# Kernel tuning notes

Hardware: AMD Instinct MI355X
Metric: run time of the kernel (lower is better)

The kernel has to match this reference:

```python
import jax, jax.numpy as jnp
import numpy as np

EPS = 1e-6

def _conv(x, w, padding):
    # x: [B,C,H,W], w: [O,I,kh,kw]
    return jax.lax.conv_general_dilated(x, w, window_strides=(1, 1), padding=padding,
                                        dimension_numbers=('NCHW', 'OIHW', 'NCHW'))

def setup_inputs() -> dict:
    key = jax.random.key(0)
    ks = jax.random.split(key, 8)
    C = 512
    B, H, W = 4, 64, 64
    s1 = 1.0 / np.sqrt(C)          # 1x1 conv fan-in
    s3 = 1.0 / np.sqrt(C * 9)      # 3x3 conv fan-in
    return {
        'x': jax.random.normal(ks[0], (B, C, H, W), dtype=jnp.float32),
        'ln_w': jnp.ones((C,), dtype=jnp.float32),
        'ln_b': jnp.zeros((C,), dtype=jnp.float32),
        'wq': jax.random.normal(ks[1], (C, C, 1, 1), dtype=jnp.float32) * s1,
        'wk': jax.random.normal(ks[2], (C, C, 3, 3), dtype=jnp.float32) * s3,
        'wv': jax.random.normal(ks[3], (C, C, 3, 3), dtype=jnp.float32) * s3,
        'wp': jax.random.normal(ks[4], (C, C, 1, 1), dtype=jnp.float32) * s1,
        'bp': jnp.zeros((C,), dtype=jnp.float32),
    }

def reference(x, ln_w, ln_b, wq, wk, wv, wp, bp):
    # channels_first LayerNorm over C
    u = jnp.mean(x, axis=1, keepdims=True)
    s = jnp.mean((x - u) ** 2, axis=1, keepdims=True)
    h = (x - u) / jnp.sqrt(s + EPS)
    h = ln_w[None, :, None, None] * h + ln_b[None, :, None, None]

    q = _conv(h, wq, 'VALID')           # 1x1
    k = _conv(h, wk, [(1, 1), (1, 1)])  # 3x3, pad 1
    v = _conv(h, wv, [(1, 1), (1, 1)])

    b, c, H, W = q.shape
    hw = H * W
    q = q.reshape(b, c, hw)
    k = k.reshape(b, c, hw)
    v = v.reshape(b, c, hw)

    scale = jnp.asarray(int(c) ** (-0.5), q.dtype)
    attn = jnp.einsum('bcm,bcn->bmn', q, k) * scale  # [b, hw_q, hw_k]
    attn = jax.nn.softmax(attn, axis=2)
    out = jnp.einsum('bcn,bmn->bcm', v, attn)        # [b, c, hw_q]
    out = out.reshape(b, c, H, W)

    out = _conv(out, wp, 'VALID') + bp[None, :, None, None]
    return x + out
```

## Files before the change

kernel.cpp:

```cpp
#include <hip/hip_runtime.h>
#include <hip/hip_bf16.h>

#define C_DIM 512
#define HW    4096
#define BATCH 4
#define PW    66
#define PPIX  (PW*PW)

typedef __attribute__((ext_vector_type(8))) short bf16x8;
typedef __attribute__((ext_vector_type(4))) float f32x4;
typedef __attribute__((ext_vector_type(16))) float f32x16;
typedef __attribute__((ext_vector_type(2))) long long l64x2;

static __device__ __forceinline__ short f2b(float f) {
    union { float f; unsigned u; } v; v.f = f;
    unsigned r = v.u + 0x7fffu + ((v.u >> 16) & 1u);
    return (short)(r >> 16);
}
static __device__ __forceinline__ float b2f(short s) {
    union { unsigned u; float f; } v; v.u = ((unsigned)(unsigned short)s) << 16;
    return v.f;
}

static __device__ __forceinline__ f32x4 zero4() {
    f32x4 v = {0.f, 0.f, 0.f, 0.f};
    return v;
}
static __device__ __forceinline__ f32x16 zero16() {
    f32x16 v = {0.f,0.f,0.f,0.f, 0.f,0.f,0.f,0.f, 0.f,0.f,0.f,0.f, 0.f,0.f,0.f,0.f};
    return v;
}

static __device__ __forceinline__ void gload16(const void* g, void* l) {
    __builtin_amdgcn_global_load_lds(
        (__attribute__((address_space(1))) void*)g,
        (__attribute__((address_space(3))) void*)l, 16, 0, 0);
}

__global__ void k_cvt_bf16(const float* __restrict__ in, short* __restrict__ out, int n) {
    int i = blockIdx.x * 256 + threadIdx.x;
    if (i < n) out[i] = f2b(in[i]);
}

__global__ void k_reorder_w3(const float* __restrict__ w, short* __restrict__ out) {
    int i = blockIdx.x * 256 + threadIdx.x;
    int c   = i & 511;
    int tap = (i >> 9) % 9;
    int o   = i / (9 * 512);
    out[i] = f2b(w[((size_t)o * 512 + c) * 9 + tap]);
}

__global__ void k_cvt_k8(const short* __restrict__ in, unsigned char* __restrict__ out) {
    int i = blockIdx.x * 256 + threadIdx.x;
    int m = i >> 6;
    int p = (i & 63) * 8;
    int kcp = p >> 6, g = (p >> 4) & 3, half = (p >> 3) & 1;
    int chb = (kcp * 2 + half) * 32 + g * 8;
    bf16x8 v = *(const bf16x8*)&in[(size_t)m * 512 + chb];
    int lo = __builtin_amdgcn_cvt_pk_fp8_f32(b2f(v[0]), b2f(v[1]), 0, false);
    lo     = __builtin_amdgcn_cvt_pk_fp8_f32(b2f(v[2]), b2f(v[3]), lo, true);
    int hi = __builtin_amdgcn_cvt_pk_fp8_f32(b2f(v[4]), b2f(v[5]), 0, false);
    hi     = __builtin_amdgcn_cvt_pk_fp8_f32(b2f(v[6]), b2f(v[7]), hi, true);
    *(uint2*)&out[(size_t)m * 512 + p] = make_uint2((unsigned)lo, (unsigned)hi);
}

__global__ void k_ln_stats(const float* __restrict__ x, float* __restrict__ mean,
                           float* __restrict__ rstd) {
    __shared__ float ss[8][32];
    __shared__ float sq2[8][32];
    int bid = blockIdx.x;
    int t = threadIdx.x;
    int px = t & 31, cg = t >> 5;
    int p = bid * 32 + px;
    int b = p >> 12, pix = p & 4095;
    const float* xp = x + (size_t)b * C_DIM * HW + pix;
    float s = 0.f, sq = 0.f;
    #pragma unroll 4
    for (int c = cg * 64; c < cg * 64 + 64; ++c) {
        float v = xp[(size_t)c * HW];
        s += v; sq += v * v;
    }
    ss[cg][px] = s;
    sq2[cg][px] = sq;
    __syncthreads();
    if (t < 32) {
        float S = 0.f, Q = 0.f;
        #pragma unroll
        for (int j = 0; j < 8; ++j) { S += ss[j][t]; Q += sq2[j][t]; }
        float mu  = S * (1.0f / C_DIM);
        float var = Q * (1.0f / C_DIM) - mu * mu;
        int pg = bid * 32 + t;
        mean[pg] = mu;
        rstd[pg] = 1.0f / sqrtf(var + 1e-6f);
    }
}

__global__ void k_ln_apply(const float* __restrict__ x, const float* __restrict__ mean,
                           const float* __restrict__ rstd, const float* __restrict__ lnw,
                           const float* __restrict__ lnb, short* __restrict__ hp) {
    __shared__ short tile[64][65];
    int bid = blockIdx.x;
    int ct = bid & 7, y = (bid >> 3) & 63, b = bid >> 9;
    int c0 = ct * 64, p0 = y * 64;
    int t = threadIdx.x;
    int pi = t & 63, ci0 = t >> 6;
    int pg = (b << 12) + p0 + pi;
    float mu = mean[pg], rs = rstd[pg];
    const float* xb = x + (size_t)b * C_DIM * HW;
    #pragma unroll
    for (int cc = 0; cc < 64; cc += 4) {
        int c = c0 + cc + ci0;
        float v = xb[(size_t)c * HW + p0 + pi];
        tile[cc + ci0][pi] = f2b((v - mu) * rs * lnw[c] + lnb[c]);
    }
    __syncthreads();
    int cj = t & 63, pj = t >> 6;
    #pragma unroll
    for (int pp = 0; pp < 64; pp += 4) {
        int pidx = pp + pj;
        size_t dst = ((size_t)b * PPIX + (size_t)(y + 1) * PW + 1 + pidx) * C_DIM + c0 + cj;
        hp[dst] = tile[cj][pidx];
    }
}

template<int TAPS, int GMODE, int EPI>
__global__ __launch_bounds__(256, 2) void k_gemm(
        const short* __restrict__ A, const short* __restrict__ Bw,
        void* __restrict__ Out, const float* __restrict__ bias,
        const float* __restrict__ resid)
{
    constexpr int K = TAPS * 512;
    constexpr int NKC = K / 64;
    __shared__ short Alds[128 * 64];
    __shared__ short Blds[128 * 64];
    int bid = blockIdx.x;
    int mt = bid & 31, nt = (bid >> 5) & 3, b = bid >> 7;
    int m0 = mt * 128, n0 = nt * 128;
    int t = threadIdx.x;
    int lane = t & 63, w = t >> 6;
    int wm = w >> 1, wn = w & 1;
    int g = lane >> 4, li = lane & 15;
    int srow = t >> 3, schunk = t & 7;
    const short* Ab = A + (GMODE == 0 ? (size_t)b * PPIX * C_DIM : (size_t)b * HW * C_DIM);

    f32x4 acc[4][4];
    #pragma unroll
    for (int i = 0; i < 4; ++i)
        #pragma unroll
        for (int j = 0; j < 4; ++j) acc[i][j] = zero4();

    for (int kc = 0; kc < NKC; ++kc) {
        int tap = (TAPS == 9) ? (kc >> 3) : 4;
        int cb  = (kc & 7) * 64;
        __syncthreads();
        #pragma unroll
        for (int r = 0; r < 4; ++r) {
            int row = r * 32 + srow;
            size_t goff;
            if (GMODE == 0) {
                int m = m0 + row;
                int yy = m >> 6, xx = m & 63;
                int pp = (yy + tap / 3) * PW + xx + (tap % 3);
                goff = (size_t)pp * C_DIM + cb + schunk * 8;
            } else {
                goff = (size_t)(m0 + row) * K + kc * 64 + schunk * 8;
            }
            gload16(Ab + goff, Alds + row * 64 + schunk * 8);
        }
        #pragma unroll
        for (int r = 0; r < 4; ++r) {
            int row = r * 32 + srow;
            size_t goff = (size_t)(n0 + row) * K + kc * 64 + schunk * 8;
            gload16(Bw + goff, Blds + row * 64 + schunk * 8);
        }
        __syncthreads();
        #pragma unroll
        for (int ks = 0; ks < 2; ++ks) {
            int koff = ks * 32 + g * 8;
            bf16x8 af[4], bfr[4];
            #pragma unroll
            for (int i = 0; i < 4; ++i)
                af[i] = *(const bf16x8*)&Alds[(wm * 64 + i * 16 + li) * 64 + koff];
            #pragma unroll
            for (int j = 0; j < 4; ++j)
                bfr[j] = *(const bf16x8*)&Blds[(wn * 64 + j * 16 + li) * 64 + koff];
            #pragma unroll
            for (int i = 0; i < 4; ++i)
                #pragma unroll
                for (int j = 0; j < 4; ++j)
                    acc[i][j] = __builtin_amdgcn_mfma_f32_16x16x32_bf16(af[i], bfr[j], acc[i][j], 0, 0, 0);
        }
    }
    #pragma unroll
    for (int fm = 0; fm < 4; ++fm) {
        #pragma unroll
        for (int fn = 0; fn < 4; ++fn) {
            int mrow = m0 + wm * 64 + fm * 16 + g * 4;
            int ncol = n0 + wn * 64 + fn * 16 + li;
            if constexpr (EPI == 0) {
                #pragma unroll
                for (int i = 0; i < 4; ++i) {
                    size_t dst = ((size_t)b * HW + mrow + i) * C_DIM + ncol;
                    ((short*)Out)[dst] = f2b(acc[fm][fn][i]);
                }
            } else if constexpr (EPI == 1) {
                size_t dst = ((size_t)b * C_DIM + ncol) * HW + mrow;
                short4 sv = make_short4(f2b(acc[fm][fn][0]), f2b(acc[fm][fn][1]),
                                        f2b(acc[fm][fn][2]), f2b(acc[fm][fn][3]));
                *(short4*)((short*)Out + dst) = sv;
            } else {
                size_t dst = ((size_t)b * C_DIM + ncol) * HW + mrow;
                float bb = bias[ncol];
                float4 xr = *(const float4*)(resid + dst);
                float4 o;
                o.x = acc[fm][fn][0] + bb + xr.x;
                o.y = acc[fm][fn][1] + bb + xr.y;
                o.z = acc[fm][fn][2] + bb + xr.z;
                o.w = acc[fm][fn][3] + bb + xr.w;
                *(float4*)((float*)Out + dst) = o;
            }
        }
    }
}

__global__ __launch_bounds__(256, 2) void k_gemm_kv(
        const short* __restrict__ A, const short* __restrict__ Bk,
        const short* __restrict__ Bv, short* __restrict__ OutK,
        short* __restrict__ OutV)
{
    constexpr int K = 4608;
    __shared__ short Alds[128 * 64];
    __shared__ short Bklds[128 * 64];
    __shared__ short Bvlds[128 * 64];
    int bid = blockIdx.x;
    int mt = bid & 31, nt = (bid >> 5) & 3, b = bid >> 7;
    int m0 = mt * 128, n0 = nt * 128;
    int t = threadIdx.x;
    int lane = t & 63, w = t >> 6;
    int wm = w >> 1, wn = w & 1;
    int g = lane >> 4, li = lane & 15;
    int srow = t >> 3, schunk = t & 7;
    const short* Ab = A + (size_t)b * PPIX * C_DIM;

    f32x4 accK[4][4], accV[4][4];
    #pragma unroll
    for (int i = 0; i < 4; ++i)
        #pragma unroll
        for (int j = 0; j < 4; ++j) { accK[i][j] = zero4(); accV[i][j] = zero4(); }

    for (int kc = 0; kc < 72; ++kc) {
        int tap = kc >> 3;
        int cb  = (kc & 7) * 64;
        __syncthreads();
        #pragma unroll
        for (int r = 0; r < 4; ++r) {
            int row = r * 32 + srow;
            int m = m0 + row;
            int yy = m >> 6, xx = m & 63;
            int pp = (yy + tap / 3) * PW + xx + (tap % 3);
            gload16(Ab + (size_t)pp * C_DIM + cb + schunk * 8, Alds + row * 64 + schunk * 8);
        }
        #pragma unroll
        for (int r = 0; r < 4; ++r) {
            int row = r * 32 + srow;
            size_t goff = (size_t)(n0 + row) * K + kc * 64 + schunk * 8;
            gload16(Bk + goff, Bklds + row * 64 + schunk * 8);
            gload16(Bv + goff, Bvlds + row * 64 + schunk * 8);
        }
        __syncthreads();
        #pragma unroll
        for (int ks = 0; ks < 2; ++ks) {
            int koff = ks * 32 + g * 8;
            bf16x8 af[4], bk[4], bv[4];
            #pragma unroll
            for (int i = 0; i < 4; ++i)
                af[i] = *(const bf16x8*)&Alds[(wm * 64 + i * 16 + li) * 64 + koff];
            #pragma unroll
            for (int j = 0; j < 4; ++j)
                bk[j] = *(const bf16x8*)&Bklds[(wn * 64 + j * 16 + li) * 64 + koff];
            #pragma unroll
            for (int i = 0; i < 4; ++i)
                #pragma unroll
                for (int j = 0; j < 4; ++j)
                    accK[i][j] = __builtin_amdgcn_mfma_f32_16x16x32_bf16(af[i], bk[j], accK[i][j], 0, 0, 0);
            #pragma unroll
            for (int j = 0; j < 4; ++j)
                bv[j] = *(const bf16x8*)&Bvlds[(wn * 64 + j * 16 + li) * 64 + koff];
            #pragma unroll
            for (int i = 0; i < 4; ++i)
                #pragma unroll
                for (int j = 0; j < 4; ++j)
                    accV[i][j] = __builtin_amdgcn_mfma_f32_16x16x32_bf16(af[i], bv[j], accV[i][j], 0, 0, 0);
        }
    }
    #pragma unroll
    for (int fm = 0; fm < 4; ++fm) {
        #pragma unroll
        for (int fn = 0; fn < 4; ++fn) {
            int mrow = m0 + wm * 64 + fm * 16 + g * 4;
            int ncol = n0 + wn * 64 + fn * 16 + li;
            #pragma unroll
            for (int i = 0; i < 4; ++i) {
                size_t dst = ((size_t)b * HW + mrow + i) * C_DIM + ncol;
                OutK[dst] = f2b(accK[fm][fn][i]);
            }
            size_t dstv = ((size_t)b * C_DIM + ncol) * HW + mrow;
            short4 sv = make_short4(f2b(accV[fm][fn][0]), f2b(accV[fm][fn][1]),
                                    f2b(accV[fm][fn][2]), f2b(accV[fm][fn][3]));
            *(short4*)(OutV + dstv) = sv;
        }
    }
}

#define KT 32
#define NTILES 64
__global__ __launch_bounds__(512, 2) void k_attn(
        const short* __restrict__ qT, const unsigned char* __restrict__ kT8,
        const short* __restrict__ vg, short* __restrict__ O0,
        short* __restrict__ O1, float* __restrict__ L0, float* __restrict__ L1)
{
    __shared__ __align__(16) short pool[73728];
    unsigned char* Kp8 = (unsigned char*)pool;
    short* Vp = pool + 16384;
    short* Pp = pool + 57344;

    int bid0 = blockIdx.x;
    int bid = (bid0 & 7) * 32 + (bid0 >> 3);
    int qt = bid & 31, ks = (bid >> 5) & 1, b = bid >> 6;
    int m0 = qt * 128;
    int t = threadIdx.x, lane = t & 63, w = t >> 6;
    int g = lane >> 4, li = lane & 15;
    int l31 = lane & 31, l5 = lane >> 5;

    const unsigned char* kb8 = kT8 + ((size_t)b * HW + (size_t)ks * 2048) * 512;
    const short* vb = vg + (size_t)b * C_DIM * HW + ks * 2048;

    long long qf8[16];
    {
        const short* qrow = qT + ((size_t)b * HW + m0 + w * 16 + li) * C_DIM;
        #pragma unroll
        for (int kc = 0; kc < 16; ++kc) {
            bf16x8 qv = *(const bf16x8*)&qrow[kc * 32 + g * 8];
            int lo = __builtin_amdgcn_cvt_pk_fp8_f32(b2f(qv[0]), b2f(qv[1]), 0, false);
            lo     = __builtin_amdgcn_cvt_pk_fp8_f32(b2f(qv[2]), b2f(qv[3]), lo, true);
            int hi = __builtin_amdgcn_cvt_pk_fp8_f32(b2f(qv[4]), b2f(qv[5]), 0, false);
            hi     = __builtin_amdgcn_cvt_pk_fp8_f32(b2f(qv[6]), b2f(qv[7]), hi, true);
            qf8[kc] = ((long long)(unsigned)hi << 32) | (unsigned)lo;
        }
    }
    f32x16 oacc[8];
    #pragma unroll
    for (int a = 0; a < 8; ++a) oacc[a] = zero16();
    float lsum = 0.f;

    const unsigned char* ksrc8 = kb8 + (size_t)(t & 31) * 512 + (t >> 5) * 16;
    int voff[5];
    #pragma unroll
    for (int r = 0; r < 5; ++r) {
        int D = r * 512 + t;
        int ch = D / 5;
        int c  = D - ch * 5;
        voff[r] = (c < 4) ? ch * 4096 + c * 8 : 0;
    }

    const float SC = 0.044194173824159216f * 1.4426950408889634f;

    auto STAGE = [&](int buf, int nt) {
        int n0 = nt * KT;
        const unsigned char* kS = ksrc8 + (size_t)n0 * 512;
        unsigned char* kD = Kp8 + buf * 16384 + t * 16;
        gload16(kS, kD);
        gload16(kS + 256, kD + 8192);
        short* vD = Vp + buf * 20480 + t * 8;
        #pragma unroll
        for (int r = 0; r < 5; ++r)
            gload16(vb + voff[r] + n0, vD + r * 4096);
    };

    STAGE(0, 0);
    asm volatile("s_waitcnt vmcnt(0)" ::: "memory");
    __builtin_amdgcn_s_barrier();
    __builtin_amdgcn_sched_barrier(0);

    int buf = 0;
    for (int nt = 0; nt < NTILES; ++nt) {
        if (nt + 1 < NTILES) STAGE(buf ^ 1, nt + 1);

        const unsigned char* kbase8 = Kp8 + buf * 16384 + g * 512 + li * 16;
        f32x4 s0[2], s1[2];
        s0[0] = zero4(); s0[1] = zero4(); s1[0] = zero4(); s1[1] = zero4();
        __builtin_amdgcn_s_setprio(1);
        #pragma unroll
        for (int kcp = 0; kcp < 8; ++kcp) {
            #pragma unroll
            for (int fn = 0; fn < 2; ++fn) {
                l64x2 kv = *(const l64x2*)&kbase8[kcp * 2048 + fn * 256];
                s0[fn] = __builtin_amdgcn_mfma_f32_16x16x32_fp8_fp8(kv[0], qf8[2 * kcp],     s0[fn], 0, 0, 0);
                s1[fn] = __builtin_amdgcn_mfma_f32_16x16x32_fp8_fp8(kv[1], qf8[2 * kcp + 1], s1[fn], 0, 0, 0);
            }
        }
        __builtin_amdgcn_s_setprio(0);
        #pragma unroll
        for (int fn = 0; fn < 2; ++fn) {
            float e0 = exp2f((s0[fn][0] + s1[fn][0]) * SC);
            float e1 = exp2f((s0[fn][1] + s1[fn][1]) * SC);
            float e2 = exp2f((s0[fn][2] + s1[fn][2]) * SC);
            float e3 = exp2f((s0[fn][3] + s1[fn][3]) * SC);
            lsum += (e0 + e1) + (e2 + e3);
            union { __hip_bfloat162 h; unsigned u; } p01, p23;
            p01.h = __float22bfloat162_rn(make_float2(e0, e1));
            p23.h = __float22bfloat162_rn(make_float2(e2, e3));
            *(uint2*)&Pp[(w * 16 + li) * 40 + fn * 16 + g * 4] = make_uint2(p01.u, p23.u);
        }

        asm volatile("s_waitcnt lgkmcnt(0)" ::: "memory");
        __builtin_amdgcn_s_barrier();
        __builtin_amdgcn_sched_barrier(0);

        const short* vbase = Vp + buf * 20480 + (size_t)w * 64 * 40;
        bf16x8 vf[2][2];
        #pragma unroll
        for (int cht = 0; cht < 2; ++cht)
            #pragma unroll
            for (int kx = 0; kx < 2; ++kx)
                vf[cht][kx] = *(const bf16x8*)&vbase[(cht * 32 + l31) * 40 + kx * 16 + l5 * 8];
        __builtin_amdgcn_s_setprio(1);
        #pragma unroll
        for (int q2 = 0; q2 < 4; ++q2) {
            #pragma unroll
            for (int kx = 0; kx < 2; ++kx) {
                bf16x8 pf = *(const bf16x8*)&Pp[(q2 * 32 + l31) * 40 + kx * 16 + l5 * 8];
                oacc[q2 * 2 + 0] = __builtin_amdgcn_mfma_f32_32x32x16_bf16(vf[0][kx], pf, oacc[q2 * 2 + 0], 0, 0, 0);
                oacc[q2 * 2 + 1] = __builtin_amdgcn_mfma_f32_32x32x16_bf16(vf[1][kx], pf, oacc[q2 * 2 + 1], 0, 0, 0);
            }
        }
        __builtin_amdgcn_s_setprio(0);

        asm volatile("s_waitcnt vmcnt(0)" ::: "memory");
        __builtin_amdgcn_s_barrier();
        __builtin_amdgcn_sched_barrier(0);
        buf ^= 1;
    }

    lsum += __shfl_xor(lsum, 16);
    lsum += __shfl_xor(lsum, 32);
    float* Lb = (ks ? L1 : L0) + (size_t)b * HW + m0 + w * 16;
    if (lane < 16) Lb[lane] = lsum;

    short* tp = pool + w * 9216;
    #pragma unroll
    for (int a = 0; a < 8; ++a) {
        int q2 = a >> 1, cht = a & 1;
        int q_l = q2 * 32 + l31;
        #pragma unroll
        for (int rq = 0; rq < 4; ++rq) {
            int chb = cht * 32 + rq * 8 + l5 * 4;
            union { __hip_bfloat162 h; unsigned u; } x01, x23;
            x01.h = __float22bfloat162_rn(make_float2(oacc[a][rq * 4 + 0], oacc[a][rq * 4 + 1]));
            x23.h = __float22bfloat162_rn(make_float2(oacc[a][rq * 4 + 2], oacc[a][rq * 4 + 3]));
            *(uint2*)&tp[q_l * 72 + chb] = make_uint2(x01.u, x23.u);
        }
    }
    asm volatile("s_waitcnt lgkmcnt(0)" ::: "memory");
    __builtin_amdgcn_sched_barrier(0);
    short* Ob = (ks ? O1 : O0) + ((size_t)b * HW + m0) * C_DIM + w * 64;
    #pragma unroll
    for (int qg = 0; qg < 16; ++qg) {
        int qr = qg * 8 + (lane >> 3);
        bf16x8 v = *(const bf16x8*)&tp[qr * 72 + (lane & 7) * 8];
        *(bf16x8*)&Ob[(size_t)qr * C_DIM + (lane & 7) * 8] = v;
    }
}

__global__ void k_att_comb(const short* __restrict__ O0, const short* __restrict__ O1,
                           const float* __restrict__ L0, const float* __restrict__ L1,
                           short* __restrict__ oatt) {
    int i = blockIdx.x * 256 + threadIdx.x;
    int row = i >> 6;
    int c0 = (i & 63) * 8;
    float r = 1.0f / (L0[row] + L1[row]);
    size_t base = (size_t)row * C_DIM + c0;
    bf16x8 a = *(const bf16x8*)&O0[base];
    bf16x8 c = *(const bf16x8*)&O1[base];
    bf16x8 o;
    #pragma unroll
    for (int j = 0; j < 8; ++j)
        o[j] = f2b((b2f(a[j]) + b2f(c[j])) * r);
    *(bf16x8*)&oatt[base] = o;
}

extern "C" void kernel_launch(void* const* d_in, const int* in_sizes, int n_in,
                              void* d_out, int out_size, void* d_ws, size_t ws_size,
                              hipStream_t stream) {
    const float* x    = (const float*)d_in[0];
    const float* ln_w = (const float*)d_in[1];
    const float* ln_b = (const float*)d_in[2];
    const float* wq   = (const float*)d_in[3];
    const float* wk   = (const float*)d_in[4];
    const float* wv   = (const float*)d_in[5];
    const float* wp   = (const float*)d_in[6];
    const float* bp   = (const float*)d_in[7];
    float* out = (float*)d_out;

    char* ws = (char*)d_ws;
    size_t off = 0;
    auto alloc = [&](size_t bytes) {
        char* p = ws + off;
        off += (bytes + 255) & ~(size_t)255;
        return p;
    };
    short* hp   = (short*)alloc((size_t)BATCH * PPIX * C_DIM * 2);
    short* wqb  = (short*)alloc((size_t)512 * 512 * 2);
    short* wkr  = (short*)alloc((size_t)512 * 4608 * 2);
    short* wvr  = (short*)alloc((size_t)512 * 4608 * 2);
    short* wpb  = (short*)alloc((size_t)512 * 512 * 2);
    short* qT   = (short*)alloc((size_t)BATCH * HW * C_DIM * 2);
    short* kT   = (short*)alloc((size_t)BATCH * HW * C_DIM * 2);
    short* vg   = (short*)alloc((size_t)BATCH * HW * C_DIM * 2);
    short* oatt = (short*)alloc((size_t)BATCH * HW * C_DIM * 2);
    float* mean = (float*)alloc((size_t)BATCH * HW * 4);
    float* rstd = (float*)alloc((size_t)BATCH * HW * 4);

    hipMemsetAsync(hp, 0, (size_t)BATCH * PPIX * C_DIM * 2, stream);
    k_cvt_bf16<<<1024, 256, 0, stream>>>(wq, wqb, 512 * 512);
    k_cvt_bf16<<<1024, 256, 0, stream>>>(wp, wpb, 512 * 512);
    k_reorder_w3<<<9216, 256, 0, stream>>>(wk, wkr);
    k_reorder_w3<<<9216, 256, 0, stream>>>(wv, wvr);
    k_ln_stats<<<512, 256, 0, stream>>>(x, mean, rstd);
    k_ln_apply<<<2048, 256, 0, stream>>>(x, mean, rstd, ln_w, ln_b, hp);

    k_gemm<1, 0, 0><<<512, 256, 0, stream>>>(hp, wqb, qT, nullptr, nullptr);
    k_gemm_kv<<<512, 256, 0, stream>>>(hp, wkr, wvr, kT, vg);

    unsigned char* kT8 = (unsigned char*)wkr;
    k_cvt_k8<<<4096, 256, 0, stream>>>(kT, kT8);

    short* Op0 = hp;
    short* Op1 = oatt;
    float* Ls0 = mean;
    float* Ls1 = rstd;
    k_attn<<<256, 512, 0, stream>>>(qT, kT8, vg, Op0, Op1, Ls0, Ls1);
    k_att_comb<<<4096, 256, 0, stream>>>(Op0, Op1, Ls0, Ls1, oatt);

    k_gemm<1, 1, 2><<<512, 256, 0, stream>>>(oatt, wpb, out, bp, x);
}
```

Baseline: 376.1 us.

## Fuse LayerNorm stats/apply and fold Q projection into KV conv GEMM

Merges the two LayerNorm kernels into one per-row kernel that computes statistics in shared memory and then writes the normalized bf16 padded tensor, avoiding the mean/rstd round trip and one launch. The Q 1x1 GEMM is folded into the KV 3x3 GEMM: during the center-tap K window the already loaded A tile is reused against the Q weights, which saves a separate pass over the activations. It also remaps block indices so the grid is traversed in a different order. The cost is more accumulator registers (a third 4x4 accumulator set) and extra LDS in the KV kernel, which may lower occupancy. The fused LN kernel also launches far fewer blocks.

```diff
diff --git a/kernel.cpp b/kernel.cpp
--- a/kernel.cpp
+++ b/kernel.cpp
@@ -64,62 +64,52 @@
     *(uint2*)&out[(size_t)m * 512 + p] = make_uint2((unsigned)lo, (unsigned)hi);
 }
 
-__global__ void k_ln_stats(const float* __restrict__ x, float* __restrict__ mean,
-                           float* __restrict__ rstd) {
-    __shared__ float ss[8][32];
-    __shared__ float sq2[8][32];
+__global__ void k_ln_fused(const float* __restrict__ x, const float* __restrict__ lnw,
+                           const float* __restrict__ lnb, short* __restrict__ hp) {
+    __shared__ float red[8][64];
+    __shared__ float mean_s[64], rstd_s[64];
+    __shared__ short tile[64][65];
     int bid = blockIdx.x;
+    int y = bid & 63, b = bid >> 6;
     int t = threadIdx.x;
-    int px = t & 31, cg = t >> 5;
-    int p = bid * 32 + px;
-    int b = p >> 12, pix = p & 4095;
-    const float* xp = x + (size_t)b * C_DIM * HW + pix;
+    int px = t & 63, cg = t >> 6;
+    const float* xb = x + (size_t)b * C_DIM * HW + (size_t)y * 64;
+
     float s = 0.f, sq = 0.f;
-    #pragma unroll 4
-    for (int c = cg * 64; c < cg * 64 + 64; ++c) {
-        float v = xp[(size_t)c * HW];
+    for (int c = cg * 128; c < cg * 128 + 128; ++c) {
+        float v = xb[(size_t)c * HW + px];
         s += v; sq += v * v;
     }
-    ss[cg][px] = s;
-    sq2[cg][px] = sq;
+    red[cg][px] = s;
+    red[4 + cg][px] = sq;
     __syncthreads();
-    if (t < 32) {
-        float S = 0.f, Q = 0.f;
-        #pragma unroll
-        for (int j = 0; j < 8; ++j) { S += ss[j][t]; Q += sq2[j][t]; }
+    if (t < 64) {
+        float S = red[0][t] + red[1][t] + red[2][t] + red[3][t];
+        float Q = red[4][t] + red[5][t] + red[6][t] + red[7][t];
         float mu  = S * (1.0f / C_DIM);
         float var = Q * (1.0f / C_DIM) - mu * mu;
-        int pg = bid * 32 + t;
-        mean[pg] = mu;
-        rstd[pg] = 1.0f / sqrtf(var + 1e-6f);
-    }
-}
-
-__global__ void k_ln_apply(const float* __restrict__ x, const float* __restrict__ mean,
-                           const float* __restrict__ rstd, const float* __restrict__ lnw,
-                           const float* __restrict__ lnb, short* __restrict__ hp) {
-    __shared__ short tile[64][65];
-    int bid = blockIdx.x;
-    int ct = bid & 7, y = (bid >> 3) & 63, b = bid >> 9;
-    int c0 = ct * 64, p0 = y * 64;
-    int t = threadIdx.x;
-    int pi = t & 63, ci0 = t >> 6;
-    int pg = (b << 12) + p0 + pi;
-    float mu = mean[pg], rs = rstd[pg];
-    const float* xb = x + (size_t)b * C_DIM * HW;
-    #pragma unroll
-    for (int cc = 0; cc < 64; cc += 4) {
-        int c = c0 + cc + ci0;
-        float v = xb[(size_t)c * HW + p0 + pi];
-        tile[cc + ci0][pi] = f2b((v - mu) * rs * lnw[c] + lnb[c]);
+        mean_s[t] = mu;
+        rstd_s[t] = 1.0f / sqrtf(var + 1e-6f);
     }
     __syncthreads();
+    float mu = mean_s[px], rs = rstd_s[px];
     int cj = t & 63, pj = t >> 6;
-    #pragma unroll
-    for (int pp = 0; pp < 64; pp += 4) {
-        int pidx = pp + pj;
-        size_t dst = ((size_t)b * PPIX + (size_t)(y + 1) * PW + 1 + pidx) * C_DIM + c0 + cj;
-        hp[dst] = tile[cj][pidx];
+    for (int ct = 0; ct < 8; ++ct) {
+        int c0 = ct * 64;
+        #pragma unroll
+        for (int cc = 0; cc < 64; cc += 4) {
+            int c = c0 + cc + cg;
+            float v = xb[(size_t)c * HW + px];
+            tile[cc + cg][px] = f2b((v - mu) * rs * lnw[c] + lnb[c]);
+        }
+        __syncthreads();
+        #pragma unroll
+        for (int pp = 0; pp < 64; pp += 4) {
+            int pidx = pp + pj;
+            size_t dst = ((size_t)b * PPIX + (size_t)(y + 1) * PW + 1 + pidx) * C_DIM + c0 + cj;
+            hp[dst] = tile[cj][pidx];
+        }
+        __syncthreads();
     }
 }
 
@@ -223,16 +213,19 @@
     }
 }
 
-__global__ __launch_bounds__(256, 2) void k_gemm_kv(
+__global__ __launch_bounds__(256, 2) void k_gemm_kvq(
         const short* __restrict__ A, const short* __restrict__ Bk,
-        const short* __restrict__ Bv, short* __restrict__ OutK,
-        short* __restrict__ OutV)
+        const short* __restrict__ Bv, const short* __restrict__ Bq,
+        short* __restrict__ OutK, short* __restrict__ OutV,
+        short* __restrict__ OutQ)
 {
     constexpr int K = 4608;
     __shared__ short Alds[128 * 64];
     __shared__ short Bklds[128 * 64];
     __shared__ short Bvlds[128 * 64];
-    int bid = blockIdx.x;
+    __shared__ short Bqlds[128 * 64];
+    int bid0 = blockIdx.x;
+    int bid = (bid0 & 7) * 64 + (bid0 >> 3);
     int mt = bid & 31, nt = (bid >> 5) & 3, b = bid >> 7;
     int m0 = mt * 128, n0 = nt * 128;
     int t = threadIdx.x;
@@ -242,15 +235,18 @@
     int srow = t >> 3, schunk = t & 7;
     const short* Ab = A + (size_t)b * PPIX * C_DIM;
 
-    f32x4 accK[4][4], accV[4][4];
+    f32x4 accK[4][4], accV[4][4], accQ[4][4];
     #pragma unroll
     for (int i = 0; i < 4; ++i)
         #pragma unroll
-        for (int j = 0; j < 4; ++j) { accK[i][j] = zero4(); accV[i][j] = zero4(); }
+        for (int j = 0; j < 4; ++j) {
+            accK[i][j] = zero4(); accV[i][j] = zero4(); accQ[i][j] = zero4();
+        }
 
     for (int kc = 0; kc < 72; ++kc) {
         int tap = kc >> 3;
         int cb  = (kc & 7) * 64;
+        bool qwin = (kc >= 32) && (kc < 40);
         __syncthreads();
         #pragma unroll
         for (int r = 0; r < 4; ++r) {
@@ -267,6 +263,14 @@
             gload16(Bk + goff, Bklds + row * 64 + schunk * 8);
             gload16(Bv + goff, Bvlds + row * 64 + schunk * 8);
         }
+        if (qwin) {
+            #pragma unroll
+            for (int r = 0; r < 4; ++r) {
+                int row = r * 32 + srow;
+                size_t goff = (size_t)(n0 + row) * 512 + (kc - 32) * 64 + schunk * 8;
+                gload16(Bq + goff, Bqlds + row * 64 + schunk * 8);
+            }
+        }
         __syncthreads();
         #pragma unroll
         for (int ks = 0; ks < 2; ++ks) {
@@ -291,6 +295,15 @@
                 #pragma unroll
                 for (int j = 0; j < 4; ++j)
                     accV[i][j] = __builtin_amdgcn_mfma_f32_16x16x32_bf16(af[i], bv[j], accV[i][j], 0, 0, 0);
+            if (qwin) {
+                #pragma unroll
+                for (int j = 0; j < 4; ++j) {
+                    bf16x8 bq = *(const bf16x8*)&Bqlds[(wn * 64 + j * 16 + li) * 64 + koff];
+                    #pragma unroll
+                    for (int i = 0; i < 4; ++i)
+                        accQ[i][j] = __builtin_amdgcn_mfma_f32_16x16x32_bf16(af[i], bq, accQ[i][j], 0, 0, 0);
+                }
+            }
         }
     }
     #pragma unroll
@@ -303,6 +316,7 @@
             for (int i = 0; i < 4; ++i) {
                 size_t dst = ((size_t)b * HW + mrow + i) * C_DIM + ncol;
                 OutK[dst] = f2b(accK[fm][fn][i]);
+                OutQ[dst] = f2b(accQ[fm][fn][i]);
             }
             size_t dstv = ((size_t)b * C_DIM + ncol) * HW + mrow;
             short4 sv = make_short4(f2b(accV[fm][fn][0]), f2b(accV[fm][fn][1]),
@@ -526,11 +540,9 @@
     k_cvt_bf16<<<1024, 256, 0, stream>>>(wp, wpb, 512 * 512);
     k_reorder_w3<<<9216, 256, 0, stream>>>(wk, wkr);
     k_reorder_w3<<<9216, 256, 0, stream>>>(wv, wvr);
-    k_ln_stats<<<512, 256, 0, stream>>>(x, mean, rstd);
-    k_ln_apply<<<2048, 256, 0, stream>>>(x, mean, rstd, ln_w, ln_b, hp);
-
-    k_gemm<1, 0, 0><<<512, 256, 0, stream>>>(hp, wqb, qT, nullptr, nullptr);
-    k_gemm_kv<<<512, 256, 0, stream>>>(hp, wkr, wvr, kT, vg);
+    k_ln_fused<<<256, 256, 0, stream>>>(x, ln_w, ln_b, hp);
+
+    k_gemm_kvq<<<512, 256, 0, stream>>>(hp, wkr, wvr, wqb, kT, vg, qT);
 
     unsigned char* kT8 = (unsigned char*)wkr;
     k_cvt_k8<<<4096, 256, 0, stream>>>(kT, kT8);
```

After: 387.0 us. 2.9% more time.
